# Performance work log

Hardware: AMD Instinct MI355X
Metric: run time of the kernel (lower is better)

## Reference

```python
import jax, jax.numpy as jnp
from jax import lax
import numpy as np

B, T, D = 16, 4096, 512          # batch, encoder length, d_model
C, FW = 10, 100                  # aconv_chans, aconv_filts (kernel width 2*FW+1)
SHARP = 2.0                      # sharpening_factor


def setup_inputs() -> dict:
    key = jax.random.key(0)
    ks = jax.random.split(key, 11)
    s = 1.0 / np.sqrt(D)
    sc = 1.0 / np.sqrt(2 * FW + 1)
    return {
        "value": jax.random.normal(ks[0], (B, T, D), jnp.float32),
        "query": jax.random.normal(ks[1], (B, D), jnp.float32),
        "input_lengths": jax.random.randint(ks[2], (B,), T // 2, T + 1),
        "att_prev": jax.random.uniform(ks[3], (B, T), jnp.float32),
        # learned parameters (torch Linear stores W as [out,in]; y = x @ W.T + b)
        "W_enc": jax.random.uniform(ks[4], (D, D), jnp.float32, -s, s),
        "b_enc": jax.random.uniform(ks[5], (D,), jnp.float32, -s, s),
        "W_dec": jax.random.uniform(ks[6], (D, D), jnp.float32, -s, s),
        "W_att": jax.random.uniform(ks[7], (D, C), jnp.float32, -s, s),
        "W_conv": jax.random.uniform(ks[8], (C, 1, 2 * FW + 1), jnp.float32, -sc, sc),
        "w_g": jax.random.uniform(ks[9], (1, D), jnp.float32, -s, s),
        "b_g": jax.random.uniform(ks[10], (1,), jnp.float32, -s, s),
    }


def reference(value, query, input_lengths, att_prev,
              W_enc, b_enc, W_dec, W_att, W_conv, w_g, b_g):
    # pre_compute_enc_h = mlp_enc(enc_h): [B,T,D]
    pre_enc = jnp.einsum('btd,ed->bte', value, W_enc) + b_enc
    # dec_z_tiled = mlp_dec(dec_z): [B,1,D]
    dec_tiled = (query @ W_dec.T)[:, None, :]
    # loc_conv: 1D conv over T, in_ch=1 -> out_ch=C, same padding -> [B,C,T]
    conv = lax.conv_general_dilated(att_prev[:, None, :], W_conv,
                                    window_strides=(1,), padding=[(FW, FW)],
                                    dimension_numbers=('NCH', 'OIH', 'NCH'))
    # mlp_att on transposed conv: [B,T,C] @ W_att.T -> [B,T,D]
    att_conv = jnp.einsum('bct,dc->btd', conv, W_att)
    # e = gvec(tanh(sum)): [B,T]
    e = jnp.einsum('btd,d->bt', jnp.tanh(att_conv + pre_enc + dec_tiled), w_g[0]) + b_g[0]
    # pad mask: positions >= length are masked to -inf (use large finite neg)
    pad_mask = jnp.arange(T)[None, :] >= input_lengths[:, None]
    e = jnp.where(pad_mask, -1e30, e)
    att_weights = jax.nn.softmax(SHARP * e, axis=1)            # [B,T]
    context = jnp.einsum('btd,bt->bd', value, att_weights)     # [B,D]
    return context, att_weights
```

## Files before the change

### kernel.cpp

```cpp
#include <hip/hip_runtime.h>
#include <hip/hip_bf16.h>

constexpr int kB  = 16;
constexpr int kT  = 4096;
constexpr int kD  = 512;
constexpr int kC  = 10;
constexpr int kFW = 100;
constexpr int kKW = 2 * kFW + 1;
constexpr int kKP = 544;

typedef __attribute__((ext_vector_type(8))) short short8_t;
typedef __attribute__((ext_vector_type(4))) float float4_t;

__device__ __forceinline__ float tanh_fast(float x) {
  float ax = fabsf(x);
  float z  = __expf(-2.0f * ax);
  float r  = (1.0f - z) / (1.0f + z);
  return copysignf(r, x);
}

__device__ __forceinline__ short f2bf(float x) {
  unsigned u = __float_as_uint(x);
  u += 0x7fffu + ((u >> 16) & 1u);
  return (short)(u >> 16);
}

__device__ __forceinline__ unsigned pk2(float lo, float hi) {
  __hip_bfloat162 h = __float22bfloat162_rn(make_float2(lo, hi));
  union { __hip_bfloat162 h2; unsigned u; } cv; cv.h2 = h; return cv.u;
}

__device__ __forceinline__ float bf2f(short s) {
  return __uint_as_float(((unsigned)(unsigned short)s) << 16);
}

__device__ __forceinline__ void glds16(const void* g, void* l) {
  __builtin_amdgcn_global_load_lds(
      (const __attribute__((address_space(1))) void*)g,
      (__attribute__((address_space(3))) void*)l, 16, 0, 0);
}

__global__ __launch_bounds__(256) void prep_kernel(
    const float* __restrict__ query, const float* __restrict__ W_dec,
    const float* __restrict__ b_enc, float* __restrict__ bias,
    const float* __restrict__ W_enc, const float* __restrict__ W_att,
    short* __restrict__ Wbf,
    const float* __restrict__ att_prev, const float* __restrict__ W_conv,
    const float* __restrict__ value, const int* __restrict__ lens,
    short* __restrict__ Abf) {
  __shared__ float ap[256 + 2 * kFW];
  __shared__ float wc[kC * kKW];
  int blk = blockIdx.x;
  int tid = threadIdx.x;

  if (blk < 2048) {
    int gw   = (blk * 256 + tid) >> 6;
    int lane = tid & 63;
    int b = gw >> 9, d = gw & (kD - 1);
    const float* q = query + (size_t)b * kD;
    const float* w = W_dec + (size_t)d * kD;
    float s = 0.f;
#pragma unroll
    for (int k0 = 0; k0 < kD; k0 += 256) {
      float4 qa = *(const float4*)(q + k0 + lane * 4);
      float4 wa = *(const float4*)(w + k0 + lane * 4);
      s += qa.x * wa.x + qa.y * wa.y + qa.z * wa.z + qa.w * wa.w;
    }
#pragma unroll
    for (int off = 32; off > 0; off >>= 1) s += __shfl_down(s, off, 64);
    if (lane == 0) bias[gw] = b_enc[d] + s;
  } else if (blk < 2048 + 512) {
    int d = blk - 2048;
    for (int c = tid; c < kKP; c += 256) {
      float v = 0.f;
      if (c < kD)           v = W_enc[(size_t)d * kD + c];
      else if (c < kD + kC) v = W_att[(size_t)d * kC + (c - kD)];
      Wbf[(size_t)d * kKP + c] = f2bf(v);
    }
  } else if (blk < 2048 + 512 + 256) {
    int lin = blk - 2560;
    int b = lin >> 4, t0 = (lin & 15) * 256;
    for (int i = tid; i < kC * kKW; i += 256) wc[i] = W_conv[i];
    for (int i = tid; i < 256 + 2 * kFW; i += 256) {
      int p = t0 - kFW + i;
      ap[i] = (p >= 0 && p < kT) ? att_prev[(size_t)b * kT + p] : 0.f;
    }
    __syncthreads();
    float acc[kC];
#pragma unroll
    for (int c = 0; c < kC; ++c) acc[c] = 0.f;
    for (int j = 0; j < kKW; ++j) {
      float a = ap[tid + j];
#pragma unroll
      for (int c = 0; c < kC; ++c) acc[c] += a * wc[c * kKW + j];
    }
    unsigned ow[16];
#pragma unroll
    for (int i = 0; i < 5; ++i) ow[i] = pk2(acc[2 * i], acc[2 * i + 1]);
#pragma unroll
    for (int i = 5; i < 16; ++i) ow[i] = 0u;
    uint4* out = (uint4*)(Abf + ((size_t)b * kT + t0 + tid) * kKP + kD);
#pragma unroll
    for (int i = 0; i < 4; ++i)
      out[i] = make_uint4(ow[4 * i], ow[4 * i + 1], ow[4 * i + 2], ow[4 * i + 3]);
  } else {
    int lin = blk - 2816;
    int b = lin >> 6, t0 = (lin & 63) * 64;
    if (t0 >= lens[b]) return;
    const float* src = value + ((size_t)b * kT + t0) * kD;
    short* dst = Abf + ((size_t)b * kT + t0) * kKP;
#pragma unroll
    for (int i = 0; i < 16; ++i) {
      int c = tid + i * 256;
      int row = c >> 6, col = (c & 63) * 8;
      float4 f0 = *(const float4*)(src + (size_t)row * kD + col);
      float4 f1 = *(const float4*)(src + (size_t)row * kD + col + 4);
      uint4 o;
      o.x = pk2(f0.x, f0.y); o.y = pk2(f0.z, f0.w);
      o.z = pk2(f1.x, f1.y); o.w = pk2(f1.z, f1.w);
      *(uint4*)(dst + (size_t)row * kKP + col) = o;
    }
  }
}

__global__ __launch_bounds__(256, 3) void e_kernel(
    const short* __restrict__ Abf, const short* __restrict__ Wbf,
    const float* __restrict__ bias, const float* __restrict__ w_g,
    const int* __restrict__ lens, float* __restrict__ e_part) {
  __shared__ short As[128 * 64];
  __shared__ short Bs[128 * 64];

  int tid = threadIdx.x;
  int L    = blockIdx.x;
  int xcd  = L & 7;
  int slot = L >> 3;
  int bn   = slot & 3;
  int mt   = (slot >> 2) * 8 + xcd;
  int b  = mt >> 5;
  int t0 = (mt & 31) * 128;
  if (t0 >= lens[b]) return;
  int n0 = bn * 128;

  int w    = tid >> 6;
  int lane = tid & 63;
  int nl   = lane & 15;
  int quad = lane >> 4;
  int wm = w >> 1, wn = w & 1;

  int r8 = lane >> 3;
  int kc = (lane & 7) ^ r8;
  const short* asrc = Abf + ((size_t)(b * kT + t0) + w * 32 + r8) * kKP + kc * 8;
  const short* bsrc = Wbf + (size_t)(n0 + w * 32 + r8) * kKP + kc * 8;
  short* adst = &As[(w * 32) * 64];
  short* bdst = &Bs[(w * 32) * 64];

  int axr = nl & 7;
  const short* aBase = &As[(wm * 64 + nl) * 64];
  const short* bBase = &Bs[(wn * 64 + nl) * 64];
  int co0 = ((0 * 4 + quad) ^ axr) * 8;
  int co1 = ((1 * 4 + quad) ^ axr) * 8;

  float4_t acc[4][4] = {};

  for (int kk = 0; kk < 8; ++kk) {
    int ko = kk * 64;
    __syncthreads();
#pragma unroll
    for (int j = 0; j < 4; ++j) {
      glds16(asrc + ko + (size_t)(j * 8) * kKP, adst + j * 8 * 64);
      glds16(bsrc + ko + (size_t)(j * 8) * kKP, bdst + j * 8 * 64);
    }
    __syncthreads();
#pragma unroll
    for (int ks = 0; ks < 2; ++ks) {
      int co = ks ? co1 : co0;
      short8_t a_frag[4], b_frag[4];
#pragma unroll
      for (int i = 0; i < 4; ++i) a_frag[i] = *(const short8_t*)(aBase + i * 1024 + co);
#pragma unroll
      for (int j = 0; j < 4; ++j) b_frag[j] = *(const short8_t*)(bBase + j * 1024 + co);
#pragma unroll
      for (int i = 0; i < 4; ++i)
#pragma unroll
        for (int j = 0; j < 4; ++j)
          acc[i][j] = __builtin_amdgcn_mfma_f32_16x16x32_bf16(
              a_frag[i], b_frag[j], acc[i][j], 0, 0, 0);
    }
  }

  {
    __syncthreads();
    int r4  = lane >> 2;
    int kc4 = (lane & 3) ^ (r4 & 3);
    const short* asrcT = Abf + ((size_t)(b * kT + t0) + w * 32 + r4) * kKP + 512 + kc4 * 8;
    const short* bsrcT = Wbf + (size_t)(n0 + w * 32 + r4) * kKP + 512 + kc4 * 8;
    short* adstT = &As[(w * 32) * 32];
    short* bdstT = &Bs[(w * 32) * 32];
    glds16(asrcT,                adstT);
    glds16(asrcT + 16 * kKP,     adstT + 16 * 32);
    glds16(bsrcT,                bdstT);
    glds16(bsrcT + 16 * kKP,     bdstT + 16 * 32);
    __syncthreads();
    int coT = (quad ^ (nl & 3)) * 8;
    const short* aBT = &As[(wm * 64 + nl) * 32];
    const short* bBT = &Bs[(wn * 64 + nl) * 32];
    short8_t a_frag[4], b_frag[4];
#pragma unroll
    for (int i = 0; i < 4; ++i) a_frag[i] = *(const short8_t*)(aBT + i * 512 + coT);
#pragma unroll
    for (int j = 0; j < 4; ++j) b_frag[j] = *(const short8_t*)(bBT + j * 512 + coT);
#pragma unroll
    for (int i = 0; i < 4; ++i)
#pragma unroll
      for (int j = 0; j < 4; ++j)
        acc[i][j] = __builtin_amdgcn_mfma_f32_16x16x32_bf16(
            a_frag[i], b_frag[j], acc[i][j], 0, 0, 0);
  }

  float bias_r[4], wg_r[4];
#pragma unroll
  for (int j = 0; j < 4; ++j) {
    int d = n0 + wn * 64 + j * 16 + nl;
    bias_r[j] = bias[b * kD + d];
    wg_r[j]   = w_g[d];
  }
  int p = wn * 4 + bn;
  float* ep = e_part + ((size_t)p * kB + b) * kT + t0 + wm * 64;
#pragma unroll
  for (int i = 0; i < 4; ++i) {
#pragma unroll
    for (int r = 0; r < 4; ++r) {
      float s = 0.f;
#pragma unroll
      for (int j = 0; j < 4; ++j)
        s += wg_r[j] * tanh_fast(acc[i][j][r] + bias_r[j]);
      s += __shfl_xor(s, 1, 64);
      s += __shfl_xor(s, 2, 64);
      s += __shfl_xor(s, 4, 64);
      s += __shfl_xor(s, 8, 64);
      if (nl == 0) ep[i * 16 + quad * 4 + r] = s;
    }
  }
}

__global__ void softmax1_kernel(const float* __restrict__ e_part,
                                const int* __restrict__ lens,
                                float* __restrict__ eb,
                                float* __restrict__ stats,
                                float* __restrict__ ctx) {
  __shared__ float sred[256];
  int b = blockIdx.x >> 4, ch = blockIdx.x & 15;
  int tid = threadIdx.x;
  int len = lens[b];
  if (ch == 0) {
    ctx[b * kD + tid]       = 0.f;
    ctx[b * kD + 256 + tid] = 0.f;
  }
  int t = ch * 256 + tid;
  float v = -3.0e38f;
  if (t < len) {
    const float* ep = e_part + (size_t)b * kT + t;
    float s = 0.f;
#pragma unroll
    for (int p = 0; p < 8; ++p) s += ep[(size_t)p * kB * kT];
    eb[(size_t)b * kT + t] = s;
    v = s;
  }
  sred[tid] = v; __syncthreads();
  for (int s = 128; s > 0; s >>= 1) {
    if (tid < s) sred[tid] = fmaxf(sred[tid], sred[tid + s]);
    __syncthreads();
  }
  float m = sred[0]; __syncthreads();
  float l = (v > -1.0e38f) ? __expf(2.0f * (v - m)) : 0.f;
  sred[tid] = l; __syncthreads();
  for (int s = 128; s > 0; s >>= 1) {
    if (tid < s) sred[tid] += sred[tid + s];
    __syncthreads();
  }
  if (tid == 0) {
    stats[(b * 16 + ch) * 2]     = m;
    stats[(b * 16 + ch) * 2 + 1] = sred[0];
  }
}

__global__ void ctx_att_kernel(const float* __restrict__ eb,
                               const float* __restrict__ stats,
                               const int* __restrict__ lens,
                               const short* __restrict__ Abf,
                               float* __restrict__ att,
                               float* __restrict__ ctx) {
  __shared__ float red[4][kD];
  int b = blockIdx.y;
  int len = lens[b];
  int t0 = blockIdx.x * 64;
  int tid = threadIdx.x;
  float M = -3.0e38f;
#pragma unroll
  for (int p = 0; p < 16; ++p) M = fmaxf(M, stats[(b * 16 + p) * 2]);
  float Lsum = 0.f;
#pragma unroll
  for (int p = 0; p < 16; ++p) {
    float mc = stats[(b * 16 + p) * 2], lc = stats[(b * 16 + p) * 2 + 1];
    if (lc > 0.f) Lsum += lc * __expf(2.0f * (mc - M));
  }
  float inv = 1.0f / Lsum;
  const float* e = eb + (size_t)b * kT + t0;
  if (tid < 64) {
    int t = t0 + tid;
    att[(size_t)b * kT + t] = (t < len) ? __expf(2.0f * (e[tid] - M)) * inv : 0.0f;
  }
  if (t0 >= len) return;
  int w = tid >> 6, lane = tid & 63;
  int tb = w * 16;
  int tmax = min(16, len - t0 - tb);
  float a[8] = {0.f, 0.f, 0.f, 0.f, 0.f, 0.f, 0.f, 0.f};
  const short* vp = Abf + ((size_t)b * kT + t0 + tb) * kKP + lane * 8;
  for (int t = 0; t < tmax; ++t) {
    float wt = __expf(2.0f * (e[tb + t] - M)) * inv;
    short8_t v = *(const short8_t*)(vp + (size_t)t * kKP);
#pragma unroll
    for (int i = 0; i < 8; ++i) a[i] += wt * bf2f(v[i]);
  }
#pragma unroll
  for (int i = 0; i < 8; ++i) red[w][lane * 8 + i] = a[i];
  __syncthreads();
  for (int col = tid; col < kD; col += 256) {
    float s = red[0][col] + red[1][col] + red[2][col] + red[3][col];
    atomicAdd(&ctx[b * kD + col], s);
  }
}

extern "C" void kernel_launch(void* const* d_in, const int* in_sizes, int n_in,
                              void* d_out, int out_size, void* d_ws, size_t ws_size,
                              hipStream_t stream) {
  const float* value    = (const float*)d_in[0];
  const float* query    = (const float*)d_in[1];
  const int*   lens     = (const int*)  d_in[2];
  const float* att_prev = (const float*)d_in[3];
  const float* W_enc    = (const float*)d_in[4];
  const float* b_enc    = (const float*)d_in[5];
  const float* W_dec    = (const float*)d_in[6];
  const float* W_att    = (const float*)d_in[7];
  const float* W_conv   = (const float*)d_in[8];
  const float* w_g      = (const float*)d_in[9];

  float* ws     = (float*)d_ws;
  float* e_part = ws;
  float* eb     = e_part + (size_t)8 * kB * kT;
  float* stats  = eb + (size_t)kB * kT;
  float* bias   = stats + 512;
  short* Wbf    = (short*)(bias + (size_t)kB * kD);
  short* Abf    = Wbf + (size_t)kD * kKP;
  float* ctx = (float*)d_out;
  float* att = ctx + (size_t)kB * kD;

  prep_kernel<<<3840, 256, 0, stream>>>(query, W_dec, b_enc, bias,
                                        W_enc, W_att, Wbf,
                                        att_prev, W_conv, value, lens, Abf);
  e_kernel<<<2048, 256, 0, stream>>>(Abf, Wbf, bias, w_g, lens, e_part);
  softmax1_kernel<<<kB * 16, 256, 0, stream>>>(e_part, lens, eb, stats, ctx);
  ctx_att_kernel<<<dim3(kT / 64, kB), 256, 0, stream>>>(eb, stats, lens, Abf, att, ctx);
}
```

Before: 284.5 us.

## Enlarge e_kernel M tile to 256 and add triple-buffered async LDS pipeline

The GEMM tile grows from 128x128 to 256x128 (8x4 MFMA accumulators per wave), which halves the grid, and the K loop now walks 17 steps of 32. Global-to-LDS loads are triple-buffered with explicit vmcnt waits so loads overlap the MFMA work, and s_setprio raises priority around the MFMA block. The register footprint roughly doubles, so launch bounds drop to 2 blocks per CU, and the e_part partition index is reordered to match.

```diff
diff --git a/kernel.cpp b/kernel.cpp
--- a/kernel.cpp
+++ b/kernel.cpp
@@ -123,12 +123,12 @@
   }
 }
 
-__global__ __launch_bounds__(256, 3) void e_kernel(
+__global__ __launch_bounds__(256, 2) void e_kernel(
     const short* __restrict__ Abf, const short* __restrict__ Wbf,
     const float* __restrict__ bias, const float* __restrict__ w_g,
     const int* __restrict__ lens, float* __restrict__ e_part) {
-  __shared__ short As[128 * 64];
-  __shared__ short Bs[128 * 64];
+  __shared__ short As[3 * 256 * 32];
+  __shared__ short Bs[3 * 128 * 32];
 
   int tid = threadIdx.x;
   int L    = blockIdx.x;
@@ -136,8 +136,8 @@
   int slot = L >> 3;
   int bn   = slot & 3;
   int mt   = (slot >> 2) * 8 + xcd;
-  int b  = mt >> 5;
-  int t0 = (mt & 31) * 128;
+  int b  = mt >> 4;
+  int t0 = (mt & 15) * 256;
   if (t0 >= lens[b]) return;
   int n0 = bn * 128;
 
@@ -147,75 +147,61 @@
   int quad = lane >> 4;
   int wm = w >> 1, wn = w & 1;
 
-  int r8 = lane >> 3;
-  int kc = (lane & 7) ^ r8;
-  const short* asrc = Abf + ((size_t)(b * kT + t0) + w * 32 + r8) * kKP + kc * 8;
-  const short* bsrc = Wbf + (size_t)(n0 + w * 32 + r8) * kKP + kc * 8;
-  short* adst = &As[(w * 32) * 64];
-  short* bdst = &Bs[(w * 32) * 64];
-
-  int axr = nl & 7;
-  const short* aBase = &As[(wm * 64 + nl) * 64];
-  const short* bBase = &Bs[(wn * 64 + nl) * 64];
-  int co0 = ((0 * 4 + quad) ^ axr) * 8;
-  int co1 = ((1 * 4 + quad) ^ axr) * 8;
-
-  float4_t acc[4][4] = {};
-
-  for (int kk = 0; kk < 8; ++kk) {
-    int ko = kk * 64;
-    __syncthreads();
-#pragma unroll
-    for (int j = 0; j < 4; ++j) {
-      glds16(asrc + ko + (size_t)(j * 8) * kKP, adst + j * 8 * 64);
-      glds16(bsrc + ko + (size_t)(j * 8) * kKP, bdst + j * 8 * 64);
-    }
-    __syncthreads();
-#pragma unroll
-    for (int ks = 0; ks < 2; ++ks) {
-      int co = ks ? co1 : co0;
-      short8_t a_frag[4], b_frag[4];
-#pragma unroll
-      for (int i = 0; i < 4; ++i) a_frag[i] = *(const short8_t*)(aBase + i * 1024 + co);
-#pragma unroll
-      for (int j = 0; j < 4; ++j) b_frag[j] = *(const short8_t*)(bBase + j * 1024 + co);
-#pragma unroll
-      for (int i = 0; i < 4; ++i)
-#pragma unroll
-        for (int j = 0; j < 4; ++j)
-          acc[i][j] = __builtin_amdgcn_mfma_f32_16x16x32_bf16(
-              a_frag[i], b_frag[j], acc[i][j], 0, 0, 0);
-    }
-  }
-
-  {
-    __syncthreads();
-    int r4  = lane >> 2;
-    int kc4 = (lane & 3) ^ (r4 & 3);
-    const short* asrcT = Abf + ((size_t)(b * kT + t0) + w * 32 + r4) * kKP + 512 + kc4 * 8;
-    const short* bsrcT = Wbf + (size_t)(n0 + w * 32 + r4) * kKP + 512 + kc4 * 8;
-    short* adstT = &As[(w * 32) * 32];
-    short* bdstT = &Bs[(w * 32) * 32];
-    glds16(asrcT,                adstT);
-    glds16(asrcT + 16 * kKP,     adstT + 16 * 32);
-    glds16(bsrcT,                bdstT);
-    glds16(bsrcT + 16 * kKP,     bdstT + 16 * 32);
-    __syncthreads();
-    int coT = (quad ^ (nl & 3)) * 8;
-    const short* aBT = &As[(wm * 64 + nl) * 32];
-    const short* bBT = &Bs[(wn * 64 + nl) * 32];
-    short8_t a_frag[4], b_frag[4];
-#pragma unroll
-    for (int i = 0; i < 4; ++i) a_frag[i] = *(const short8_t*)(aBT + i * 512 + coT);
-#pragma unroll
-    for (int j = 0; j < 4; ++j) b_frag[j] = *(const short8_t*)(bBT + j * 512 + coT);
-#pragma unroll
-    for (int i = 0; i < 4; ++i)
+  int r4  = lane >> 2;
+  int kc4 = (lane & 3) ^ (r4 & 3);
+  const short* asrc = Abf + ((size_t)(b * kT + t0) + w * 64 + r4) * kKP + kc4 * 8;
+  const short* bsrc = Wbf + (size_t)(n0 + w * 32 + r4) * kKP + kc4 * 8;
+
+  int co = (quad ^ (nl & 3)) * 8;
+
+  float4_t acc[8][4] = {};
+
+#define STAGE(bi, k0)                                                   \
+  do {                                                                  \
+    short* ad = As + (bi) * 8192 + (w * 64) * 32;                       \
+    short* bd = Bs + (bi) * 4096 + (w * 32) * 32;                       \
+    const short* as_ = asrc + (k0);                                     \
+    const short* bs_ = bsrc + (k0);                                     \
+    glds16(as_,                ad);                                     \
+    glds16(as_ + 16 * kKP,     ad + 16 * 32);                           \
+    glds16(as_ + 32 * kKP,     ad + 32 * 32);                           \
+    glds16(as_ + 48 * kKP,     ad + 48 * 32);                           \
+    glds16(bs_,                bd);                                     \
+    glds16(bs_ + 16 * kKP,     bd + 16 * 32);                           \
+  } while (0)
+
+  STAGE(0, 0);
+  STAGE(1, 32);
+  int cur = 0, stg = 2;
+#pragma unroll 1
+  for (int kk = 0; kk < 17; ++kk) {
+    if (kk < 15) STAGE(stg, (kk + 2) * 32);
+    if (kk < 15)      asm volatile("s_waitcnt vmcnt(12)" ::: "memory");
+    else if (kk < 16) asm volatile("s_waitcnt vmcnt(6)" ::: "memory");
+    else              asm volatile("s_waitcnt vmcnt(0)" ::: "memory");
+    __builtin_amdgcn_s_barrier();
+    __builtin_amdgcn_sched_barrier(0);
+    const short* aB = As + cur * 8192 + (wm * 128 + nl) * 32 + co;
+    const short* bB = Bs + cur * 4096 + (wn * 64 + nl) * 32 + co;
+    short8_t a_frag[8], b_frag[4];
+#pragma unroll
+    for (int i = 0; i < 8; ++i) a_frag[i] = *(const short8_t*)(aB + i * 512);
+#pragma unroll
+    for (int j = 0; j < 4; ++j) b_frag[j] = *(const short8_t*)(bB + j * 512);
+    __builtin_amdgcn_s_setprio(1);
+#pragma unroll
+    for (int i = 0; i < 8; ++i)
 #pragma unroll
       for (int j = 0; j < 4; ++j)
         acc[i][j] = __builtin_amdgcn_mfma_f32_16x16x32_bf16(
             a_frag[i], b_frag[j], acc[i][j], 0, 0, 0);
-  }
+    __builtin_amdgcn_s_setprio(0);
+    __builtin_amdgcn_sched_barrier(0);
+    __builtin_amdgcn_s_barrier();
+    cur = (cur == 2) ? 0 : cur + 1;
+    stg = (stg == 2) ? 0 : stg + 1;
+  }
+#undef STAGE
 
   float bias_r[4], wg_r[4];
 #pragma unroll
@@ -224,10 +210,10 @@
     bias_r[j] = bias[b * kD + d];
     wg_r[j]   = w_g[d];
   }
-  int p = wn * 4 + bn;
-  float* ep = e_part + ((size_t)p * kB + b) * kT + t0 + wm * 64;
-#pragma unroll
-  for (int i = 0; i < 4; ++i) {
+  int p = bn * 2 + wn;
+  float* ep = e_part + ((size_t)p * kB + b) * kT + t0 + wm * 128;
+#pragma unroll
+  for (int i = 0; i < 8; ++i) {
 #pragma unroll
     for (int r = 0; r < 4; ++r) {
       float s = 0.f;
@@ -358,7 +344,7 @@
   prep_kernel<<<3840, 256, 0, stream>>>(query, W_dec, b_enc, bias,
                                         W_enc, W_att, Wbf,
                                         att_prev, W_conv, value, lens, Abf);
-  e_kernel<<<2048, 256, 0, stream>>>(Abf, Wbf, bias, w_g, lens, e_part);
+  e_kernel<<<1024, 256, 0, stream>>>(Abf, Wbf, bias, w_g, lens, e_part);
   softmax1_kernel<<<kB * 16, 256, 0, stream>>>(e_part, lens, eb, stats, ctx);
   ctx_att_kernel<<<dim3(kT / 64, kB), 256, 0, stream>>>(eb, stats, lens, Abf, att, ctx);
 }
```

Measured after the change: 306.1 us. 7.6% more time.

## Replace context atomics with partial buffers and reorder prep blocks

Applied to the files above, without the earlier changes.

Each ctx_att block now writes its partial context row to a workspace buffer, and a new small kernel sums the 64 partials per batch. This replaces the float atomicAdd contention and makes the result deterministic, at the cost of one extra launch and extra traffic. The prep kernel is also reordered so the value-to-bf16 conversion blocks come first and use 32 rows each instead of 64. This spreads the heavy work over more blocks scheduled early.

```diff
diff --git a/kernel.cpp b/kernel.cpp
--- a/kernel.cpp
+++ b/kernel.cpp
@@ -54,63 +54,12 @@
   int tid = threadIdx.x;
 
   if (blk < 2048) {
-    int gw   = (blk * 256 + tid) >> 6;
-    int lane = tid & 63;
-    int b = gw >> 9, d = gw & (kD - 1);
-    const float* q = query + (size_t)b * kD;
-    const float* w = W_dec + (size_t)d * kD;
-    float s = 0.f;
-#pragma unroll
-    for (int k0 = 0; k0 < kD; k0 += 256) {
-      float4 qa = *(const float4*)(q + k0 + lane * 4);
-      float4 wa = *(const float4*)(w + k0 + lane * 4);
-      s += qa.x * wa.x + qa.y * wa.y + qa.z * wa.z + qa.w * wa.w;
-    }
-#pragma unroll
-    for (int off = 32; off > 0; off >>= 1) s += __shfl_down(s, off, 64);
-    if (lane == 0) bias[gw] = b_enc[d] + s;
-  } else if (blk < 2048 + 512) {
-    int d = blk - 2048;
-    for (int c = tid; c < kKP; c += 256) {
-      float v = 0.f;
-      if (c < kD)           v = W_enc[(size_t)d * kD + c];
-      else if (c < kD + kC) v = W_att[(size_t)d * kC + (c - kD)];
-      Wbf[(size_t)d * kKP + c] = f2bf(v);
-    }
-  } else if (blk < 2048 + 512 + 256) {
-    int lin = blk - 2560;
-    int b = lin >> 4, t0 = (lin & 15) * 256;
-    for (int i = tid; i < kC * kKW; i += 256) wc[i] = W_conv[i];
-    for (int i = tid; i < 256 + 2 * kFW; i += 256) {
-      int p = t0 - kFW + i;
-      ap[i] = (p >= 0 && p < kT) ? att_prev[(size_t)b * kT + p] : 0.f;
-    }
-    __syncthreads();
-    float acc[kC];
-#pragma unroll
-    for (int c = 0; c < kC; ++c) acc[c] = 0.f;
-    for (int j = 0; j < kKW; ++j) {
-      float a = ap[tid + j];
-#pragma unroll
-      for (int c = 0; c < kC; ++c) acc[c] += a * wc[c * kKW + j];
-    }
-    unsigned ow[16];
-#pragma unroll
-    for (int i = 0; i < 5; ++i) ow[i] = pk2(acc[2 * i], acc[2 * i + 1]);
-#pragma unroll
-    for (int i = 5; i < 16; ++i) ow[i] = 0u;
-    uint4* out = (uint4*)(Abf + ((size_t)b * kT + t0 + tid) * kKP + kD);
-#pragma unroll
-    for (int i = 0; i < 4; ++i)
-      out[i] = make_uint4(ow[4 * i], ow[4 * i + 1], ow[4 * i + 2], ow[4 * i + 3]);
-  } else {
-    int lin = blk - 2816;
-    int b = lin >> 6, t0 = (lin & 63) * 64;
+    int b = blk >> 7, t0 = (blk & 127) * 32;
     if (t0 >= lens[b]) return;
     const float* src = value + ((size_t)b * kT + t0) * kD;
     short* dst = Abf + ((size_t)b * kT + t0) * kKP;
 #pragma unroll
-    for (int i = 0; i < 16; ++i) {
+    for (int i = 0; i < 8; ++i) {
       int c = tid + i * 256;
       int row = c >> 6, col = (c & 63) * 8;
       float4 f0 = *(const float4*)(src + (size_t)row * kD + col);
@@ -120,6 +69,56 @@
       o.z = pk2(f1.x, f1.y); o.w = pk2(f1.z, f1.w);
       *(uint4*)(dst + (size_t)row * kKP + col) = o;
     }
+  } else if (blk < 2048 + 256) {
+    int lin = blk - 2048;
+    int b = lin >> 4, t0 = (lin & 15) * 256;
+    for (int i = tid; i < kC * kKW; i += 256) wc[i] = W_conv[i];
+    for (int i = tid; i < 256 + 2 * kFW; i += 256) {
+      int p = t0 - kFW + i;
+      ap[i] = (p >= 0 && p < kT) ? att_prev[(size_t)b * kT + p] : 0.f;
+    }
+    __syncthreads();
+    float acc[kC];
+#pragma unroll
+    for (int c = 0; c < kC; ++c) acc[c] = 0.f;
+    for (int j = 0; j < kKW; ++j) {
+      float a = ap[tid + j];
+#pragma unroll
+      for (int c = 0; c < kC; ++c) acc[c] += a * wc[c * kKW + j];
+    }
+    unsigned ow[16];
+#pragma unroll
+    for (int i = 0; i < 5; ++i) ow[i] = pk2(acc[2 * i], acc[2 * i + 1]);
+#pragma unroll
+    for (int i = 5; i < 16; ++i) ow[i] = 0u;
+    uint4* out = (uint4*)(Abf + ((size_t)b * kT + t0 + tid) * kKP + kD);
+#pragma unroll
+    for (int i = 0; i < 4; ++i)
+      out[i] = make_uint4(ow[4 * i], ow[4 * i + 1], ow[4 * i + 2], ow[4 * i + 3]);
+  } else if (blk < 2048 + 256 + 512) {
+    int d = blk - 2304;
+    for (int c = tid; c < kKP; c += 256) {
+      float v = 0.f;
+      if (c < kD)           v = W_enc[(size_t)d * kD + c];
+      else if (c < kD + kC) v = W_att[(size_t)d * kC + (c - kD)];
+      Wbf[(size_t)d * kKP + c] = f2bf(v);
+    }
+  } else {
+    int gw   = ((blk - 2816) * 256 + tid) >> 6;
+    int lane = tid & 63;
+    int b = gw >> 9, d = gw & (kD - 1);
+    const float* q = query + (size_t)b * kD;
+    const float* w = W_dec + (size_t)d * kD;
+    float s = 0.f;
+#pragma unroll
+    for (int k0 = 0; k0 < kD; k0 += 256) {
+      float4 qa = *(const float4*)(q + k0 + lane * 4);
+      float4 wa = *(const float4*)(w + k0 + lane * 4);
+      s += qa.x * wa.x + qa.y * wa.y + qa.z * wa.z + qa.w * wa.w;
+    }
+#pragma unroll
+    for (int off = 32; off > 0; off >>= 1) s += __shfl_down(s, off, 64);
+    if (lane == 0) bias[gw] = b_enc[d] + s;
   }
 }
 
@@ -246,16 +245,11 @@
 __global__ void softmax1_kernel(const float* __restrict__ e_part,
                                 const int* __restrict__ lens,
                                 float* __restrict__ eb,
-                                float* __restrict__ stats,
-                                float* __restrict__ ctx) {
+                                float* __restrict__ stats) {
   __shared__ float sred[256];
   int b = blockIdx.x >> 4, ch = blockIdx.x & 15;
   int tid = threadIdx.x;
   int len = lens[b];
-  if (ch == 0) {
-    ctx[b * kD + tid]       = 0.f;
-    ctx[b * kD + 256 + tid] = 0.f;
-  }
   int t = ch * 256 + tid;
   float v = -3.0e38f;
   if (t < len) {
@@ -289,12 +283,13 @@
                                const int* __restrict__ lens,
                                const short* __restrict__ Abf,
                                float* __restrict__ att,
-                               float* __restrict__ ctx) {
+                               float* __restrict__ ctx_part) {
   __shared__ float red[4][kD];
   int b = blockIdx.y;
   int len = lens[b];
   int t0 = blockIdx.x * 64;
   int tid = threadIdx.x;
+  float* cp = ctx_part + ((size_t)b * 64 + blockIdx.x) * kD;
   float M = -3.0e38f;
 #pragma unroll
   for (int p = 0; p < 16; ++p) M = fmaxf(M, stats[(b * 16 + p) * 2]);
@@ -310,7 +305,10 @@
     int t = t0 + tid;
     att[(size_t)b * kT + t] = (t < len) ? __expf(2.0f * (e[tid] - M)) * inv : 0.0f;
   }
-  if (t0 >= len) return;
+  if (t0 >= len) {
+    cp[tid] = 0.f; cp[tid + 256] = 0.f;
+    return;
+  }
   int w = tid >> 6, lane = tid & 63;
   int tb = w * 16;
   int tmax = min(16, len - t0 - tb);
@@ -327,8 +325,19 @@
   __syncthreads();
   for (int col = tid; col < kD; col += 256) {
     float s = red[0][col] + red[1][col] + red[2][col] + red[3][col];
-    atomicAdd(&ctx[b * kD + col], s);
-  }
+    cp[col] = s;
+  }
+}
+
+__global__ void ctx_reduce_kernel(const float* __restrict__ ctx_part,
+                                  float* __restrict__ ctx) {
+  int b = blockIdx.x;
+  int col = threadIdx.x;
+  const float* cp = ctx_part + (size_t)b * 64 * kD + col;
+  float s = 0.f;
+#pragma unroll 8
+  for (int c = 0; c < 64; ++c) s += cp[(size_t)c * kD];
+  ctx[b * kD + col] = s;
 }
 
 extern "C" void kernel_launch(void* const* d_in, const int* in_sizes, int n_in,
@@ -350,15 +359,17 @@
   float* eb     = e_part + (size_t)8 * kB * kT;
   float* stats  = eb + (size_t)kB * kT;
   float* bias   = stats + 512;
-  short* Wbf    = (short*)(bias + (size_t)kB * kD);
+  float* ctxp   = bias + (size_t)kB * kD;
+  short* Wbf    = (short*)(ctxp + (size_t)kB * 64 * kD);
   short* Abf    = Wbf + (size_t)kD * kKP;
   float* ctx = (float*)d_out;
   float* att = ctx + (size_t)kB * kD;
 
-  prep_kernel<<<3840, 256, 0, stream>>>(query, W_dec, b_enc, bias,
+  prep_kernel<<<4864, 256, 0, stream>>>(query, W_dec, b_enc, bias,
                                         W_enc, W_att, Wbf,
                                         att_prev, W_conv, value, lens, Abf);
   e_kernel<<<2048, 256, 0, stream>>>(Abf, Wbf, bias, w_g, lens, e_part);
-  softmax1_kernel<<<kB * 16, 256, 0, stream>>>(e_part, lens, eb, stats, ctx);
-  ctx_att_kernel<<<dim3(kT / 64, kB), 256, 0, stream>>>(eb, stats, lens, Abf, att, ctx);
-}
+  softmax1_kernel<<<kB * 16, 256, 0, stream>>>(e_part, lens, eb, stats);
+  ctx_att_kernel<<<dim3(kT / 64, kB), 256, 0, stream>>>(eb, stats, lens, Abf, att, ctxp);
+  ctx_reduce_kernel<<<kB, kD, 0, stream>>>(ctxp, ctx);
+}
```

New measurement: 297.1 us. +4.4%, slower.
